# Kernel optimization log

Hardware: AMD Instinct MI355X
Metric: run time of the kernel (lower is better)

The kernel has to match this reference:

```python
import jax, jax.numpy as jnp
import numpy as np

N = 16777216
NC = 262144

def setup_inputs() -> dict:
    key = jax.random.key(0)
    k1, k2 = jax.random.split(key)
    site_energy = jax.random.normal(k1, (N, 1), dtype=jnp.float32)
    segment_ids = jnp.sort(jax.random.randint(k2, (N,), 0, NC, dtype=jnp.int64))
    return {"site_energy": site_energy, "segment_ids": segment_ids, "num_crystals": NC}

def reference(site_energy, segment_ids, num_crystals):
    flat = site_energy.squeeze(-1)                                   # [N]
    total = jax.ops.segment_sum(flat, segment_ids, num_segments=num_crystals)
    counts = jax.ops.segment_sum(jnp.ones_like(flat), segment_ids, num_segments=num_crystals)
    return (total / jnp.maximum(counts, 1.0))[:, None]               # [nc,1]
```

## Files before the change

kernel.cpp:

```cpp
#include <hip/hip_runtime.h>
#include <hip/hip_bf16.h>


#define VPT 8

__global__ void seg_sum_kernel(const float* __restrict__ x,
                               const void* __restrict__ seg,
                               float* __restrict__ sums,
                               float* __restrict__ cnts,
                               int n) {
    const int* s32 = (const int*)seg;
    const long long* s64 = (const long long*)seg;
    const bool is64 = (s32[n - 1] == 0);

    const long long base = (long long)(blockIdx.x * (long long)blockDim.x + threadIdx.x) * VPT;
    const int lane = threadIdx.x & 63;

    int ids[VPT];
    float vals[VPT];
    int nv = 0;
    if (base < n) {
        long long rem = (long long)n - base;
        nv = (rem >= VPT) ? VPT : (int)rem;
    }

    if (nv == VPT) {
        const float4* xv = (const float4*)(x + base);
        float4 a = xv[0], b = xv[1];
        vals[0] = a.x; vals[1] = a.y; vals[2] = a.z; vals[3] = a.w;
        vals[4] = b.x; vals[5] = b.y; vals[6] = b.z; vals[7] = b.w;
        if (is64) {
            const longlong2* iv = (const longlong2*)(s64 + base);
            #pragma unroll
            for (int k = 0; k < 4; ++k) {
                longlong2 t = iv[k];
                ids[2 * k]     = (int)t.x;
                ids[2 * k + 1] = (int)t.y;
            }
        } else {
            const int4* iv = (const int4*)(s32 + base);
            int4 t0 = iv[0], t1 = iv[1];
            ids[0] = t0.x; ids[1] = t0.y; ids[2] = t0.z; ids[3] = t0.w;
            ids[4] = t1.x; ids[5] = t1.y; ids[6] = t1.z; ids[7] = t1.w;
        }
    } else {
        #pragma unroll
        for (int k = 0; k < VPT; ++k) {
            if (k < nv) {
                ids[k]  = is64 ? (int)s64[base + k] : s32[base + k];
                vals[k] = x[base + k];
            } else {
                ids[k]  = -1;
                vals[k] = 0.0f;
            }
        }
    }

    int   cur = (nv > 0) ? ids[0] : -1;
    float s   = (nv > 0) ? vals[0] : 0.0f;
    float c   = (nv > 0) ? 1.0f : 0.0f;
    #pragma unroll
    for (int k = 1; k < VPT; ++k) {
        if (k < nv) {
            if (ids[k] == cur) {
                s += vals[k];
                c += 1.0f;
            } else {
                atomicAdd(&sums[cur], s);
                atomicAdd(&cnts[cur], c);
                cur = ids[k];
                s = vals[k];
                c = 1.0f;
            }
        }
    }

    int lid = cur;
    #pragma unroll
    for (int off = 1; off < 64; off <<= 1) {
        float os = __shfl_up(s, off);
        float oc = __shfl_up(c, off);
        int  oid = __shfl_up(lid, off);
        if (lane >= off && oid == lid) {
            s += os;
            c += oc;
        }
    }

    int nid = __shfl_down(lid, 1);
    bool emit = (lid >= 0) && ((lane == 63) || (nid != lid));
    if (emit) {
        atomicAdd(&sums[lid], s);
        atomicAdd(&cnts[lid], c);
    }
}

__global__ void finalize_kernel(float* __restrict__ out,
                                const float* __restrict__ cnts,
                                int nc) {
    int cidx = blockIdx.x * blockDim.x + threadIdx.x;
    if (cidx < nc) {
        out[cidx] = out[cidx] / fmaxf(cnts[cidx], 1.0f);
    }
}

extern "C" void kernel_launch(void* const* d_in, const int* in_sizes, int n_in,
                              void* d_out, int out_size, void* d_ws, size_t ws_size,
                              hipStream_t stream) {
    const float* x = (const float*)d_in[0];
    const void* seg = d_in[1];
    const int n = in_sizes[0];
    const int nc = out_size;

    float* sums = (float*)d_out;
    float* cnts = (float*)d_ws;

    hipMemsetAsync(sums, 0, (size_t)nc * sizeof(float), stream);
    hipMemsetAsync(cnts, 0, (size_t)nc * sizeof(float), stream);

    const int block = 256;
    const long long elems_per_block = (long long)block * VPT;
    const int grid = (int)((n + elems_per_block - 1) / elems_per_block);
    seg_sum_kernel<<<grid, block, 0, stream>>>(x, seg, sums, cnts, n);

    const int fgrid = (nc + block - 1) / block;
    finalize_kernel<<<fgrid, block, 0, stream>>>(sums, cnts, nc);
}
```

Before: 41.54 us.

## Stage segment ids through LDS with direct global-to-LDS loads

Segment ids are now loaded cooperatively per block into shared memory using global_load_lds (buffer loads straight to LDS). Each thread then reads its 8 ids from LDS, and the tail block falls back to scalar loads. The per-thread vector loads of int64 ids are replaced, and the two memsets are merged into one over a workspace holding both sums and counts. This adds a 16KB LDS buffer, a barrier, and strided LDS reads that may bank-conflict. The total bytes read from global memory are unchanged.

Result: no change. 41.30 us (-0.6%).

```diff
diff --git a/kernel.cpp b/kernel.cpp
--- a/kernel.cpp
+++ b/kernel.cpp
@@ -2,105 +2,152 @@
 #include <hip/hip_bf16.h>
 
 
+#define BLOCK 256
 #define VPT 8
+#define CHUNK (BLOCK * VPT)
+#define NWAVES (BLOCK / 64)
 
-__global__ void seg_sum_kernel(const float* __restrict__ x,
-                               const void* __restrict__ seg,
-                               float* __restrict__ sums,
-                               float* __restrict__ cnts,
-                               int n) {
+typedef float fx4 __attribute__((ext_vector_type(4)));
+typedef const __attribute__((address_space(1))) unsigned int gas_u32;
+typedef __attribute__((address_space(3))) unsigned int las_u32;
+
+__global__ __launch_bounds__(BLOCK)
+void seg_sum_kernel(const float* __restrict__ x,
+                    const void* __restrict__ seg,
+                    float* __restrict__ gsums,
+                    float* __restrict__ gcnts,
+                    int n) {
+    __shared__ int lid[CHUNK * 2];
+
     const int* s32 = (const int*)seg;
-    const long long* s64 = (const long long*)seg;
     const bool is64 = (s32[n - 1] == 0);
 
-    const long long base = (long long)(blockIdx.x * (long long)blockDim.x + threadIdx.x) * VPT;
-    const int lane = threadIdx.x & 63;
+    const int tid = threadIdx.x;
+    const int wave = tid >> 6;
+    const int lane = tid & 63;
+    const long long bbase = (long long)blockIdx.x * CHUNK;
 
-    int ids[VPT];
+    {
+        const char* segb = (const char*)seg;
+        const int eb = is64 ? 8 : 4;
+        const long long gbytes_lo  = bbase * eb;
+        const long long gbytes_end = (long long)n * eb;
+        const int ops = (CHUNK / 1024) * eb * (1024 / 16) / 64;
+        for (int op = wave; op < ops; op += NWAVES) {
+            long long goff = gbytes_lo + (long long)op * 1024 + (long long)lane * 16;
+            long long gmax = gbytes_end - 16;
+            if (goff > gmax) goff = gmax;
+            if (goff < 0) goff = 0;
+            __builtin_amdgcn_global_load_lds(
+                (gas_u32*)(segb + goff),
+                (las_u32*)((char*)lid + (size_t)op * 1024),
+                16, 0, 0);
+        }
+    }
+
     float vals[VPT];
+    const long long base = bbase + (long long)tid * VPT;
     int nv = 0;
     if (base < n) {
         long long rem = (long long)n - base;
         nv = (rem >= VPT) ? VPT : (int)rem;
     }
-
     if (nv == VPT) {
-        const float4* xv = (const float4*)(x + base);
-        float4 a = xv[0], b = xv[1];
+        const fx4* xv = (const fx4*)(x + base);
+        fx4 a = xv[0], b = xv[1];
         vals[0] = a.x; vals[1] = a.y; vals[2] = a.z; vals[3] = a.w;
         vals[4] = b.x; vals[5] = b.y; vals[6] = b.z; vals[7] = b.w;
-        if (is64) {
-            const longlong2* iv = (const longlong2*)(s64 + base);
-            #pragma unroll
-            for (int k = 0; k < 4; ++k) {
-                longlong2 t = iv[k];
-                ids[2 * k]     = (int)t.x;
-                ids[2 * k + 1] = (int)t.y;
-            }
-        } else {
-            const int4* iv = (const int4*)(s32 + base);
-            int4 t0 = iv[0], t1 = iv[1];
-            ids[0] = t0.x; ids[1] = t0.y; ids[2] = t0.z; ids[3] = t0.w;
-            ids[4] = t1.x; ids[5] = t1.y; ids[6] = t1.z; ids[7] = t1.w;
-        }
     } else {
         #pragma unroll
-        for (int k = 0; k < VPT; ++k) {
-            if (k < nv) {
-                ids[k]  = is64 ? (int)s64[base + k] : s32[base + k];
-                vals[k] = x[base + k];
+        for (int k = 0; k < VPT; ++k)
+            vals[k] = (k < nv) ? x[base + k] : 0.0f;
+    }
+
+    if (bbase + CHUNK > (long long)n) {
+        __syncthreads();
+        for (long long p = bbase + tid; p < bbase + CHUNK; p += BLOCK) {
+            int li = (int)(p - bbase);
+            if (p < (long long)n) {
+                if (is64) lid[li * 2] = (int)((const long long*)seg)[p];
+                else      lid[li]     = s32[p];
             } else {
-                ids[k]  = -1;
-                vals[k] = 0.0f;
+                if (is64) lid[li * 2] = -1;
+                else      lid[li]     = -1;
             }
         }
     }
+    __syncthreads();
 
-    int   cur = (nv > 0) ? ids[0] : -1;
-    float s   = (nv > 0) ? vals[0] : 0.0f;
-    float c   = (nv > 0) ? 1.0f : 0.0f;
+    int ids_[VPT];
     #pragma unroll
-    for (int k = 1; k < VPT; ++k) {
-        if (k < nv) {
-            if (ids[k] == cur) {
-                s += vals[k];
-                c += 1.0f;
-            } else {
-                atomicAdd(&sums[cur], s);
-                atomicAdd(&cnts[cur], c);
-                cur = ids[k];
-                s = vals[k];
-                c = 1.0f;
+    for (int k = 0; k < VPT; ++k) {
+        int li = tid * VPT + k;
+        ids_[k] = is64 ? lid[li * 2] : lid[li];
+        if (k >= nv) ids_[k] = -1;
+    }
+
+    if (nv > 0) {
+        int   cur = ids_[0];
+        float s   = vals[0];
+        float c   = 1.0f;
+        #pragma unroll
+        for (int k = 1; k < VPT; ++k) {
+            if (k < nv) {
+                if (ids_[k] == cur) {
+                    s += vals[k];
+                    c += 1.0f;
+                } else {
+                    atomicAdd(&gsums[cur], s);
+                    atomicAdd(&gcnts[cur], c);
+                    cur = ids_[k];
+                    s = vals[k];
+                    c = 1.0f;
+                }
             }
         }
-    }
 
-    int lid = cur;
-    #pragma unroll
-    for (int off = 1; off < 64; off <<= 1) {
-        float os = __shfl_up(s, off);
-        float oc = __shfl_up(c, off);
-        int  oid = __shfl_up(lid, off);
-        if (lane >= off && oid == lid) {
-            s += os;
-            c += oc;
+        int lid_ = cur;
+        #pragma unroll
+        for (int off = 1; off < 64; off <<= 1) {
+            float os = __shfl_up(s, off);
+            float oc = __shfl_up(c, off);
+            int  oid = __shfl_up(lid_, off);
+            if (lane >= off && oid == lid_) {
+                s += os;
+                c += oc;
+            }
         }
-    }
-
-    int nid = __shfl_down(lid, 1);
-    bool emit = (lid >= 0) && ((lane == 63) || (nid != lid));
-    if (emit) {
-        atomicAdd(&sums[lid], s);
-        atomicAdd(&cnts[lid], c);
+        int nid = __shfl_down(lid_, 1);
+        bool emit = (lane == 63) || (nid != lid_);
+        if (emit) {
+            atomicAdd(&gsums[lid_], s);
+            atomicAdd(&gcnts[lid_], c);
+        }
+    } else {
+        int lid_ = -1;
+        float s = 0.0f, c = 0.0f;
+        #pragma unroll
+        for (int off = 1; off < 64; off <<= 1) {
+            float os = __shfl_up(s, off);
+            float oc = __shfl_up(c, off);
+            int  oid = __shfl_up(lid_, off);
+            if (lane >= off && oid == lid_) {
+                s += os;
+                c += oc;
+            }
+        }
+        (void)__shfl_down(lid_, 1);
     }
 }
 
 __global__ void finalize_kernel(float* __restrict__ out,
-                                const float* __restrict__ cnts,
+                                const float* __restrict__ gsums,
+                                const float* __restrict__ gcnts,
                                 int nc) {
-    int cidx = blockIdx.x * blockDim.x + threadIdx.x;
-    if (cidx < nc) {
-        out[cidx] = out[cidx] / fmaxf(cnts[cidx], 1.0f);
+    int c = blockIdx.x * blockDim.x + threadIdx.x;
+    if (c < nc) {
+        float cv = gcnts[c];
+        out[c] = (cv > 0.0f) ? (gsums[c] / cv) : 0.0f;
     }
 }
 
@@ -112,17 +159,15 @@
     const int n = in_sizes[0];
     const int nc = out_size;
 
-    float* sums = (float*)d_out;
-    float* cnts = (float*)d_ws;
+    float* gsums = (float*)d_ws;
+    float* gcnts = (float*)d_ws + nc;
+    float* out   = (float*)d_out;
 
-    hipMemsetAsync(sums, 0, (size_t)nc * sizeof(float), stream);
-    hipMemsetAsync(cnts, 0, (size_t)nc * sizeof(float), stream);
+    (void)hipMemsetAsync(gsums, 0, (size_t)2 * nc * sizeof(float), stream);
 
-    const int block = 256;
-    const long long elems_per_block = (long long)block * VPT;
-    const int grid = (int)((n + elems_per_block - 1) / elems_per_block);
-    seg_sum_kernel<<<grid, block, 0, stream>>>(x, seg, sums, cnts, n);
+    const int grid = (int)(((long long)n + CHUNK - 1) / CHUNK);
+    seg_sum_kernel<<<grid, BLOCK, 0, stream>>>(x, seg, gsums, gcnts, n);
 
-    const int fgrid = (nc + block - 1) / block;
-    finalize_kernel<<<fgrid, block, 0, stream>>>(sums, cnts, nc);
+    const int fgrid = (nc + BLOCK - 1) / BLOCK;
+    finalize_kernel<<<fgrid, BLOCK, 0, stream>>>(out, gsums, gcnts, nc);
 }
```
